# Kernel optimization log

Measured on AMD Instinct MI355X. Metric: run time of the kernel, lower is better.

## Reference

```python
import jax, jax.numpy as jnp
import numpy as np

NEG_SLOPE = 0.01  # F.leaky_relu default


def gcn_conv(x, src, dst, W, b):
    """PyG GCNConv: add self-loops, symmetric D^-1/2 (A+I) D^-1/2 normalization."""
    N = x.shape[0]
    loops = jnp.arange(N, dtype=src.dtype)
    src_f = jnp.concatenate([src, loops])  # [E+N]
    dst_f = jnp.concatenate([dst, loops])
    # degree counted on target nodes (includes self-loop), >= 1
    deg = jax.ops.segment_sum(jnp.ones_like(dst_f, dtype=x.dtype), dst_f, num_segments=N)
    dis = jax.lax.rsqrt(deg)  # deg >= 1 so finite
    norm = dis[src_f] * dis[dst_f]  # [E+N]
    h = x @ W  # [N, F_out] linear first (PyG order)
    msg = h[src_f] * norm[:, None]
    out = jax.ops.segment_sum(msg, dst_f, num_segments=N)
    return out + b


def setup_inputs() -> dict:
    key = jax.random.key(0)
    ks = jax.random.split(key, 8)
    N, E = 10000, 320000
    F_in, F1, F2 = 512, 256, 128
    x = jax.random.normal(ks[0], (N, F_in), dtype=jnp.float32)
    edge_index = jax.random.randint(ks[1], (2, E), 0, N, dtype=jnp.int32)
    batch = jnp.zeros((N,), dtype=jnp.int32)
    # Glorot-style params
    W1 = jax.random.normal(ks[2], (F_in, F1), dtype=jnp.float32) * (1.0 / np.sqrt(F_in))
    b1 = jnp.zeros((F1,), dtype=jnp.float32)
    W2 = jax.random.normal(ks[3], (F1, F2), dtype=jnp.float32) * (1.0 / np.sqrt(F1))
    b2 = jnp.zeros((F2,), dtype=jnp.float32)
    return {"x": x, "edge_index": edge_index, "batch": batch,
            "W1": W1, "b1": b1, "W2": W2, "b2": b2}


def reference(x, edge_index, batch, W1, b1, W2, b2):
    src, dst = edge_index[0], edge_index[1]
    h = jax.nn.leaky_relu(gcn_conv(x, src, dst, W1, b1), NEG_SLOPE)
    # dropout is eval-mode identity
    h = jax.nn.leaky_relu(gcn_conv(h, src, dst, W2, b2), NEG_SLOPE)
    x1 = jax.nn.sigmoid(h @ h.T)  # [N, N] dense decode
    return (x1, h)
```

## Files before the change

### kernel.cpp

```cpp
#include <hip/hip_runtime.h>
#include <math.h>

#define LEAKY 0.01f

using short8   = __attribute__((ext_vector_type(8))) short;
using f32x4    = __attribute__((ext_vector_type(4))) float;
using ushort4e = __attribute__((ext_vector_type(4))) unsigned short;

__device__ __forceinline__ ushort f2bf(float f) {
  uint u = __float_as_uint(f);
  uint r = (u + 0x7FFFu + ((u >> 16) & 1u)) >> 16;
  return (ushort)r;
}
__device__ __forceinline__ float bf2f(ushort h) {
  uint u = ((uint)h) << 16;
  return __uint_as_float(u);
}


__global__ void k_zero_i(int* __restrict__ p, int n) {
  int i = blockIdx.x * blockDim.x + threadIdx.x;
  if (i < n) p[i] = 0;
}

__global__ void k_count(const int* __restrict__ dst, int* __restrict__ cnt, int E) {
  int i = blockIdx.x * blockDim.x + threadIdx.x;
  if (i < E) atomicAdd(&cnt[dst[i]], 1);
}

__global__ void k_scan(const int* __restrict__ cnt, int* __restrict__ rowstart,
                       int* __restrict__ cursor, float* __restrict__ dinv,
                       int N, int Etot) {
  __shared__ int part[1024];
  const int t = threadIdx.x;
  const int CH = 16;
  int base = t * CH;
  int local[CH];
  int s = 0;
#pragma unroll
  for (int i = 0; i < CH; i++) {
    int v = (base + i < N) ? cnt[base + i] : 0;
    if (base + i < N) dinv[base + i] = rsqrtf((float)v + 1.0f);
    local[i] = s;
    s += v;
  }
  part[t] = s;
  __syncthreads();
  for (int off = 1; off < 1024; off <<= 1) {
    int add = (t >= off) ? part[t - off] : 0;
    __syncthreads();
    part[t] += add;
    __syncthreads();
  }
  int excl = (t == 0) ? 0 : part[t - 1];
#pragma unroll
  for (int i = 0; i < CH; i++) {
    if (base + i < N) {
      int rs = excl + local[i];
      rowstart[base + i] = rs;
      cursor[base + i] = rs;
    }
  }
  if (t == 0) rowstart[N] = Etot;
}

__global__ void k_csr(const int* __restrict__ src, const int* __restrict__ dst,
                      int* __restrict__ cursor, int* __restrict__ esrc, int E) {
  int i = blockIdx.x * blockDim.x + threadIdx.x;
  if (i < E) {
    int d = dst[i];
    int pos = atomicAdd(&cursor[d], 1);
    esrc[pos] = src[i];
  }
}


__global__ void k_xb(const float* __restrict__ X, ushort* __restrict__ Xb, long total) {
  long i = ((long)blockIdx.x * blockDim.x + threadIdx.x) * 4;
  if (i < total) {
    float4 v = *reinterpret_cast<const float4*>(&X[i]);
    ushort4e u = {f2bf(v.x), f2bf(v.y), f2bf(v.z), f2bf(v.w)};
    *reinterpret_cast<ushort4e*>(&Xb[i]) = u;
  }
}

__global__ void k_wt(const float* __restrict__ W1, ushort* __restrict__ Wt1,
                     int K1, int N1,
                     const float* __restrict__ W2, ushort* __restrict__ Wt2,
                     int K2, int N2) {
  int i = blockIdx.x * blockDim.x + threadIdx.x;
  int t1 = K1 * N1;
  if (i < t1) {
    int k = i / N1, n = i % N1;
    Wt1[(long)n * K1 + k] = f2bf(W1[i]);
  } else if (i < t1 + K2 * N2) {
    int j = i - t1;
    int k = j / N2, n = j % N2;
    Wt2[(long)n * K2 + k] = f2bf(W2[j]);
  }
}

template <int F, int VL, bool LAST>
__global__ __launch_bounds__(64) void k_agg(const ushort* __restrict__ hlin,
                                            const float* __restrict__ dinv,
                                            const int* __restrict__ rowstart,
                                            const int* __restrict__ esrc,
                                            const float* __restrict__ bias,
                                            ushort* __restrict__ aggb,
                                            float* __restrict__ outh, int N) {
  const int node = blockIdx.x;
  const int t = threadIdx.x;
  const float di = dinv[node];
  float acc[VL];
  {
    const ushort* p = hlin + (long)node * F + t * VL;
    if constexpr (VL == 4) {
      ushort4e v = *reinterpret_cast<const ushort4e*>(p);
#pragma unroll
      for (int i = 0; i < 4; i++) acc[i] = bf2f(v[i]) * di * di;
    } else {
      uint v = *reinterpret_cast<const uint*>(p);
      acc[0] = bf2f((ushort)(v & 0xffff)) * di * di;
      acc[1] = bf2f((ushort)(v >> 16)) * di * di;
    }
  }
  const int e0 = rowstart[node], e1 = rowstart[node + 1];
  int e = e0;
  for (; e + 3 < e1; e += 4) {
    int s0 = esrc[e], s1 = esrc[e + 1], s2 = esrc[e + 2], s3 = esrc[e + 3];
    float nm0 = dinv[s0] * di, nm1 = dinv[s1] * di;
    float nm2 = dinv[s2] * di, nm3 = dinv[s3] * di;
    const ushort* p0 = hlin + (long)s0 * F + t * VL;
    const ushort* p1 = hlin + (long)s1 * F + t * VL;
    const ushort* p2 = hlin + (long)s2 * F + t * VL;
    const ushort* p3 = hlin + (long)s3 * F + t * VL;
    if constexpr (VL == 4) {
      ushort4e v0 = *reinterpret_cast<const ushort4e*>(p0);
      ushort4e v1 = *reinterpret_cast<const ushort4e*>(p1);
      ushort4e v2 = *reinterpret_cast<const ushort4e*>(p2);
      ushort4e v3 = *reinterpret_cast<const ushort4e*>(p3);
#pragma unroll
      for (int i = 0; i < 4; i++)
        acc[i] += bf2f(v0[i]) * nm0 + bf2f(v1[i]) * nm1 +
                  bf2f(v2[i]) * nm2 + bf2f(v3[i]) * nm3;
    } else {
      uint v0 = *reinterpret_cast<const uint*>(p0);
      uint v1 = *reinterpret_cast<const uint*>(p1);
      uint v2 = *reinterpret_cast<const uint*>(p2);
      uint v3 = *reinterpret_cast<const uint*>(p3);
      acc[0] += bf2f((ushort)(v0 & 0xffff)) * nm0 + bf2f((ushort)(v1 & 0xffff)) * nm1 +
                bf2f((ushort)(v2 & 0xffff)) * nm2 + bf2f((ushort)(v3 & 0xffff)) * nm3;
      acc[1] += bf2f((ushort)(v0 >> 16)) * nm0 + bf2f((ushort)(v1 >> 16)) * nm1 +
                bf2f((ushort)(v2 >> 16)) * nm2 + bf2f((ushort)(v3 >> 16)) * nm3;
    }
  }
  for (; e < e1; e++) {
    int s0 = esrc[e];
    float nm0 = dinv[s0] * di;
    const ushort* p0 = hlin + (long)s0 * F + t * VL;
    if constexpr (VL == 4) {
      ushort4e v0 = *reinterpret_cast<const ushort4e*>(p0);
#pragma unroll
      for (int i = 0; i < 4; i++) acc[i] += bf2f(v0[i]) * nm0;
    } else {
      uint v0 = *reinterpret_cast<const uint*>(p0);
      acc[0] += bf2f((ushort)(v0 & 0xffff)) * nm0;
      acc[1] += bf2f((ushort)(v0 >> 16)) * nm0;
    }
  }
#pragma unroll
  for (int i = 0; i < VL; i++) {
    float v = acc[i] + bias[t * VL + i];
    acc[i] = (v > 0.f) ? v : (LEAKY * v);
  }
  if constexpr (VL == 4) {
    ushort4e o = {f2bf(acc[0]), f2bf(acc[1]), f2bf(acc[2]), f2bf(acc[3])};
    *reinterpret_cast<ushort4e*>(&aggb[(long)node * F + t * 4]) = o;
    if constexpr (LAST) {
      float4 fo = make_float4(acc[0], acc[1], acc[2], acc[3]);
      *reinterpret_cast<float4*>(&outh[(long)node * F + t * 4]) = fo;
    }
  } else {
    uint o = (uint)f2bf(acc[0]) | ((uint)f2bf(acc[1]) << 16);
    *reinterpret_cast<uint*>(&aggb[(long)node * F + t * 2]) = o;
    if constexpr (LAST) {
      float2 fo = make_float2(acc[0], acc[1]);
      *reinterpret_cast<float2*>(&outh[(long)node * F + t * 2]) = fo;
    }
  }
}

template <int BM>
__global__ __launch_bounds__(256) void k_gemm_bt(const ushort* __restrict__ Ab,
                                                 const ushort* __restrict__ Bb,
                                                 ushort* __restrict__ Cb,
                                                 int M, int N, int K, int ldc) {
  constexpr int MI = BM / 32;
  __shared__ __align__(16) ushort lds[(BM + 128) * 128];
  ushort* ldsA = lds;
  ushort* ldsB = lds + BM * 128;

  const int tid = threadIdx.x;
  const int lane = tid & 63;
  const int wv = tid >> 6;
  const int wr = wv >> 1, wc = wv & 1;
  const long bm = (long)blockIdx.y * BM;
  const long bn = (long)blockIdx.x * 128;

  f32x4 acc[MI][4];
#pragma unroll
  for (int i = 0; i < MI; i++)
#pragma unroll
    for (int j = 0; j < 4; j++) acc[i][j] = (f32x4){0.f, 0.f, 0.f, 0.f};

  const int kb = ((lane >> 4) << 4);

  for (int k0 = 0; k0 < K; k0 += 128) {
#pragma unroll
    for (int it = 0; it < BM / 16; it++) {
      int off = it * 4096 + tid * 16;
      int row = off >> 8;
      int cb = off & 255;
      long gr = bm + row;
      uint4 v = make_uint4(0u, 0u, 0u, 0u);
      if (gr < M) v = *reinterpret_cast<const uint4*>(&Ab[gr * K + k0 + (cb >> 1)]);
      int sb = (row << 8) | (cb ^ ((row & 7) << 4));
      *reinterpret_cast<uint4*>((char*)ldsA + sb) = v;
    }
#pragma unroll
    for (int it = 0; it < 8; it++) {
      int off = it * 4096 + tid * 16;
      int row = off >> 8;
      int cb = off & 255;
      long gn = bn + row;
      uint4 v = make_uint4(0u, 0u, 0u, 0u);
      if (gn < N) v = *reinterpret_cast<const uint4*>(&Bb[gn * K + k0 + (cb >> 1)]);
      int sb = (row << 8) | (cb ^ ((row & 7) << 4));
      *reinterpret_cast<uint4*>((char*)ldsB + sb) = v;
    }
    __syncthreads();

#pragma unroll
    for (int ks = 0; ks < 4; ks++) {
      short8 af[MI], bfr[4];
#pragma unroll
      for (int mi = 0; mi < MI; mi++) {
        int row = wr * (BM / 2) + mi * 16 + (lane & 15);
        int b = ks * 64 + kb;
        int addr = (row << 8) | (b ^ ((row & 7) << 4));
        af[mi] = *reinterpret_cast<const short8*>((const char*)ldsA + addr);
      }
#pragma unroll
      for (int ni = 0; ni < 4; ni++) {
        int row = wc * 64 + ni * 16 + (lane & 15);
        int b = ks * 64 + kb;
        int addr = (row << 8) | (b ^ ((row & 7) << 4));
        bfr[ni] = *reinterpret_cast<const short8*>((const char*)ldsB + addr);
      }
#pragma unroll
      for (int mi = 0; mi < MI; mi++)
#pragma unroll
        for (int ni = 0; ni < 4; ni++)
          acc[mi][ni] = __builtin_amdgcn_mfma_f32_16x16x32_bf16(af[mi], bfr[ni], acc[mi][ni], 0, 0, 0);
    }
    __syncthreads();
  }

#pragma unroll
  for (int ni = 0; ni < 4; ni++) {
    long col = bn + wc * 64 + ni * 16 + (lane & 15);
    if (col >= N) continue;
#pragma unroll
    for (int mi = 0; mi < MI; mi++) {
      long rbase2 = bm + wr * (BM / 2) + mi * 16 + ((lane >> 4) << 2);
#pragma unroll
      for (int j = 0; j < 4; j++) {
        long row = rbase2 + j;
        if (row >= M) continue;
        Cb[row * ldc + col] = f2bf(acc[mi][ni][j]);
      }
    }
  }
}

__global__ __launch_bounds__(256) void k_decode_sym(const ushort* __restrict__ Hb,
                                                    float* __restrict__ C, int N) {
  __shared__ __align__(16) ushort lds[2 * 128 * 128];
  ushort* ldsA = lds;
  ushort* ldsB = lds + 128 * 128;

  const int tid = threadIdx.x;
  const int lane = tid & 63;
  const int wv = tid >> 6;
  const int wr = wv >> 1, wc = wv & 1;

  int t = blockIdx.x;
  int bi = (int)((sqrtf(8.f * (float)t + 1.f) - 1.f) * 0.5f);
  while ((bi + 1) * (bi + 2) / 2 <= t) bi++;
  while (bi * (bi + 1) / 2 > t) bi--;
  int bj = t - bi * (bi + 1) / 2;
  const long bm = (long)bi * 128;
  const long bn = (long)bj * 128;

#pragma unroll
  for (int s = 0; s < 2; s++) {
    long rbase = s ? bn : bm;
    ushort* L = s ? ldsB : ldsA;
#pragma unroll
    for (int it = 0; it < 8; it++) {
      int off = it * 4096 + tid * 16;
      int row = off >> 8;
      int cb = off & 255;
      long grow = rbase + row;
      uint4 v = make_uint4(0u, 0u, 0u, 0u);
      if (grow < N)
        v = *reinterpret_cast<const uint4*>(&Hb[grow * 128 + (cb >> 1)]);
      int sb = (row << 8) | (cb ^ ((row & 7) << 4));
      *reinterpret_cast<uint4*>((char*)L + sb) = v;
    }
  }
  __syncthreads();

  f32x4 acc[4][4];
#pragma unroll
  for (int i = 0; i < 4; i++)
#pragma unroll
    for (int j = 0; j < 4; j++) acc[i][j] = (f32x4){0.f, 0.f, 0.f, 0.f};

  const int kb = ((lane >> 4) << 4);
#pragma unroll
  for (int ks = 0; ks < 4; ks++) {
    short8 af[4], bfr[4];
#pragma unroll
    for (int mi = 0; mi < 4; mi++) {
      int row = wr * 64 + mi * 16 + (lane & 15);
      int b = ks * 64 + kb;
      int addr = (row << 8) | (b ^ ((row & 7) << 4));
      af[mi] = *reinterpret_cast<const short8*>((const char*)ldsA + addr);
    }
#pragma unroll
    for (int ni = 0; ni < 4; ni++) {
      int row = wc * 64 + ni * 16 + (lane & 15);
      int b = ks * 64 + kb;
      int addr = (row << 8) | (b ^ ((row & 7) << 4));
      bfr[ni] = *reinterpret_cast<const short8*>((const char*)ldsB + addr);
    }
#pragma unroll
    for (int mi = 0; mi < 4; mi++)
#pragma unroll
      for (int ni = 0; ni < 4; ni++)
        acc[mi][ni] = __builtin_amdgcn_mfma_f32_16x16x32_bf16(af[mi], bfr[ni], acc[mi][ni], 0, 0, 0);
  }

#pragma unroll
  for (int mi = 0; mi < 4; mi++)
#pragma unroll
    for (int ni = 0; ni < 4; ni++)
#pragma unroll
      for (int j = 0; j < 4; j++)
        acc[mi][ni][j] = __builtin_amdgcn_rcpf(1.f + __expf(-acc[mi][ni][j]));

  if (bi != bj) {
#pragma unroll
    for (int ni = 0; ni < 4; ni++) {
      long gr = bn + wc * 64 + ni * 16 + (lane & 15);
#pragma unroll
      for (int mi = 0; mi < 4; mi++) {
        long gc = bm + wr * 64 + mi * 16 + ((lane >> 4) << 2);
        if (gr < N && gc < N)
          __builtin_nontemporal_store(acc[mi][ni],
                                      reinterpret_cast<f32x4*>(&C[gr * N + gc]));
      }
    }
  }

  __syncthreads();

  float* ft = (float*)lds;
#pragma unroll
  for (int ni = 0; ni < 4; ni++) {
    int col = wc * 64 + ni * 16 + (lane & 15);
#pragma unroll
    for (int mi = 0; mi < 4; mi++) {
      int rb = wr * 64 + mi * 16 + ((lane >> 4) << 2);
#pragma unroll
      for (int j = 0; j < 4; j++) {
        int row = rb + j;
        int byte = (row << 9) + (col << 2);
        byte ^= ((row & 7) << 4);
        *reinterpret_cast<float*>((char*)ft + byte) = acc[mi][ni][j];
      }
    }
  }
  __syncthreads();

#pragma unroll
  for (int it = 0; it < 16; it++) {
    int r = (tid >> 5) + it * 8;
    int ch = tid & 31;
    int byte = (r << 9) + (ch << 4);
    byte ^= ((r & 7) << 4);
    f32x4 v = *reinterpret_cast<const f32x4*>((const char*)ft + byte);
    long gr = bm + r;
    long gc = bn + ch * 4;
    if (gr < N && gc < N)
      __builtin_nontemporal_store(v, reinterpret_cast<f32x4*>(&C[gr * N + gc]));
  }
}


extern "C" void kernel_launch(void* const* d_in, const int* in_sizes, int n_in,
                              void* d_out, int out_size, void* d_ws, size_t ws_size,
                              hipStream_t stream) {
  const float* x  = (const float*)d_in[0];
  const int*   ei = (const int*)d_in[1];
  const float* W1 = (const float*)d_in[3];
  const float* b1 = (const float*)d_in[4];
  const float* W2 = (const float*)d_in[5];
  const float* b2 = (const float*)d_in[6];

  const int N   = in_sizes[2];
  const int E   = in_sizes[1] / 2;
  const int Fin = in_sizes[0] / N;
  const int F1  = in_sizes[4];
  const int F2  = in_sizes[6];

  const int* src = ei;
  const int* dst = ei + E;

  float* ws = (float*)d_ws;
  ushort* w1t      = (ushort*)ws;
  ushort* w2t      = (ushort*)(ws + 65536);
  ushort* xb       = (ushort*)(ws + 81920);
  ushort* h1b      = (ushort*)(ws + 2641920);
  ushort* agg1b    = (ushort*)(ws + 3921920);
  ushort* h2b      = (ushort*)(ws + 5201920);
  ushort* hb       = (ushort*)(ws + 5841920);
  float*  dinv     = ws + 6481920;
  int*    cnt      = (int*)(ws + 6492160);
  int*    cursor   = (int*)(ws + 6502400);
  int*    rowstart = (int*)(ws + 6512640);
  int*    esrc     = (int*)(ws + 6523136);

  float* out_x1 = (float*)d_out;
  float* out_h  = out_x1 + (long)N * N;

  k_zero_i<<<(N + 255) / 256, 256, 0, stream>>>(cnt, N);
  k_count<<<(E + 255) / 256, 256, 0, stream>>>(dst, cnt, E);
  k_scan<<<1, 1024, 0, stream>>>(cnt, rowstart, cursor, dinv, N, E);
  k_csr<<<(E + 255) / 256, 256, 0, stream>>>(src, dst, cursor, esrc, E);

  {
    int tot = Fin * F1 + F1 * F2;
    k_wt<<<(tot + 255) / 256, 256, 0, stream>>>(W1, w1t, Fin, F1, W2, w2t, F1, F2);
    long xtot = (long)N * Fin;
    k_xb<<<(unsigned)((xtot / 4 + 255) / 256), 256, 0, stream>>>(x, xb, xtot);
  }

  {
    dim3 grid(F1 / 128, (N + 63) / 64);
    k_gemm_bt<64><<<grid, 256, 0, stream>>>(xb, w1t, h1b, N, F1, Fin, F1);
  }
  k_agg<256, 4, false><<<N, 64, 0, stream>>>(h1b, dinv, rowstart, esrc, b1,
                                             agg1b, nullptr, N);

  {
    dim3 grid(F2 / 128, (N + 63) / 64);
    k_gemm_bt<64><<<grid, 256, 0, stream>>>(agg1b, w2t, h2b, N, F2, F1, F2);
  }
  k_agg<128, 2, true><<<N, 64, 0, stream>>>(h2b, dinv, rowstart, esrc, b2,
                                            hb, out_h, N);

  {
    int NB = (N + 127) / 128;
    int nblk = NB * (NB + 1) / 2;
    k_decode_sym<<<nblk, 256, 0, stream>>>(hb, out_x1, N);
  }
}
```

Before: 252.5 us.

## Precompute edge norms in CSR build, merge prep kernels, widen aggregation blocks

The CSR build now also stores a per-edge normalization (dinv[src]*dinv[dst]) in CSR order, so aggregation reads one float per edge instead of gathering dinv per neighbor. The X cast and weight-transpose kernels are merged into one launch, and the zeroing kernel is replaced by hipMemsetAsync. The aggregation kernel is reworked to use 2-feature lanes with multiple waves per node for the 256-wide layer and an 8-way unroll. This adds an E-sized float buffer and more threads per block in layer 1, but the dense decode likely dominates total time.

```diff
diff --git a/kernel.cpp b/kernel.cpp
--- a/kernel.cpp
+++ b/kernel.cpp
@@ -17,11 +17,6 @@
   return __uint_as_float(u);
 }
 
-
-__global__ void k_zero_i(int* __restrict__ p, int n) {
-  int i = blockIdx.x * blockDim.x + threadIdx.x;
-  if (i < n) p[i] = 0;
-}
 
 __global__ void k_count(const int* __restrict__ dst, int* __restrict__ cnt, int E) {
   int i = blockIdx.x * blockDim.x + threadIdx.x;
@@ -65,128 +60,96 @@
 }
 
 __global__ void k_csr(const int* __restrict__ src, const int* __restrict__ dst,
-                      int* __restrict__ cursor, int* __restrict__ esrc, int E) {
+                      const float* __restrict__ dinv, int* __restrict__ cursor,
+                      int* __restrict__ esrc, float* __restrict__ enorm, int E) {
   int i = blockIdx.x * blockDim.x + threadIdx.x;
   if (i < E) {
     int d = dst[i];
+    int s = src[i];
     int pos = atomicAdd(&cursor[d], 1);
-    esrc[pos] = src[i];
-  }
-}
-
-
-__global__ void k_xb(const float* __restrict__ X, ushort* __restrict__ Xb, long total) {
-  long i = ((long)blockIdx.x * blockDim.x + threadIdx.x) * 4;
-  if (i < total) {
-    float4 v = *reinterpret_cast<const float4*>(&X[i]);
+    esrc[pos] = s;
+    enorm[pos] = dinv[s] * dinv[d];
+  }
+}
+
+__global__ void k_prep(const float* __restrict__ X, ushort* __restrict__ Xb, long xq,
+                       const float* __restrict__ W1, ushort* __restrict__ Wt1,
+                       int K1, int N1,
+                       const float* __restrict__ W2, ushort* __restrict__ Wt2,
+                       int K2, int N2) {
+  long i = (long)blockIdx.x * blockDim.x + threadIdx.x;
+  if (i < xq) {
+    long b = i * 4;
+    float4 v = *reinterpret_cast<const float4*>(&X[b]);
     ushort4e u = {f2bf(v.x), f2bf(v.y), f2bf(v.z), f2bf(v.w)};
-    *reinterpret_cast<ushort4e*>(&Xb[i]) = u;
-  }
-}
-
-__global__ void k_wt(const float* __restrict__ W1, ushort* __restrict__ Wt1,
-                     int K1, int N1,
-                     const float* __restrict__ W2, ushort* __restrict__ Wt2,
-                     int K2, int N2) {
-  int i = blockIdx.x * blockDim.x + threadIdx.x;
-  int t1 = K1 * N1;
-  if (i < t1) {
-    int k = i / N1, n = i % N1;
-    Wt1[(long)n * K1 + k] = f2bf(W1[i]);
-  } else if (i < t1 + K2 * N2) {
-    int j = i - t1;
-    int k = j / N2, n = j % N2;
-    Wt2[(long)n * K2 + k] = f2bf(W2[j]);
-  }
-}
-
-template <int F, int VL, bool LAST>
-__global__ __launch_bounds__(64) void k_agg(const ushort* __restrict__ hlin,
-                                            const float* __restrict__ dinv,
-                                            const int* __restrict__ rowstart,
-                                            const int* __restrict__ esrc,
-                                            const float* __restrict__ bias,
-                                            ushort* __restrict__ aggb,
-                                            float* __restrict__ outh, int N) {
+    *reinterpret_cast<ushort4e*>(&Xb[b]) = u;
+  } else {
+    long j = i - xq;
+    int t1 = K1 * N1;
+    if (j < t1) {
+      int k = (int)(j / N1), n = (int)(j % N1);
+      Wt1[(long)n * K1 + k] = f2bf(W1[j]);
+    } else if (j < t1 + (long)K2 * N2) {
+      long jj = j - t1;
+      int k = (int)(jj / N2), n = (int)(jj % N2);
+      Wt2[(long)n * K2 + k] = f2bf(W2[jj]);
+    }
+  }
+}
+
+template <int F, int WAVES, bool LAST>
+__global__ __launch_bounds__(64 * WAVES) void k_agg(const ushort* __restrict__ hlin,
+                                                    const float* __restrict__ dinv,
+                                                    const int* __restrict__ rowstart,
+                                                    const int* __restrict__ esrc,
+                                                    const float* __restrict__ enorm,
+                                                    const float* __restrict__ bias,
+                                                    ushort* __restrict__ aggb,
+                                                    float* __restrict__ outh, int N) {
+  constexpr int FS = F / WAVES;
   const int node = blockIdx.x;
-  const int t = threadIdx.x;
+  const int tid = threadIdx.x;
+  const int w = tid >> 6;
+  const int lane = tid & 63;
+  const int f0 = w * FS + lane * 2;
   const float di = dinv[node];
-  float acc[VL];
+
+  float acc0, acc1;
   {
-    const ushort* p = hlin + (long)node * F + t * VL;
-    if constexpr (VL == 4) {
-      ushort4e v = *reinterpret_cast<const ushort4e*>(p);
-#pragma unroll
-      for (int i = 0; i < 4; i++) acc[i] = bf2f(v[i]) * di * di;
-    } else {
-      uint v = *reinterpret_cast<const uint*>(p);
-      acc[0] = bf2f((ushort)(v & 0xffff)) * di * di;
-      acc[1] = bf2f((ushort)(v >> 16)) * di * di;
-    }
+    uint v = *reinterpret_cast<const uint*>(&hlin[(long)node * F + f0]);
+    float dd = di * di;
+    acc0 = bf2f((ushort)(v & 0xffff)) * dd;
+    acc1 = bf2f((ushort)(v >> 16)) * dd;
   }
   const int e0 = rowstart[node], e1 = rowstart[node + 1];
   int e = e0;
-  for (; e + 3 < e1; e += 4) {
-    int s0 = esrc[e], s1 = esrc[e + 1], s2 = esrc[e + 2], s3 = esrc[e + 3];
-    float nm0 = dinv[s0] * di, nm1 = dinv[s1] * di;
-    float nm2 = dinv[s2] * di, nm3 = dinv[s3] * di;
-    const ushort* p0 = hlin + (long)s0 * F + t * VL;
-    const ushort* p1 = hlin + (long)s1 * F + t * VL;
-    const ushort* p2 = hlin + (long)s2 * F + t * VL;
-    const ushort* p3 = hlin + (long)s3 * F + t * VL;
-    if constexpr (VL == 4) {
-      ushort4e v0 = *reinterpret_cast<const ushort4e*>(p0);
-      ushort4e v1 = *reinterpret_cast<const ushort4e*>(p1);
-      ushort4e v2 = *reinterpret_cast<const ushort4e*>(p2);
-      ushort4e v3 = *reinterpret_cast<const ushort4e*>(p3);
-#pragma unroll
-      for (int i = 0; i < 4; i++)
-        acc[i] += bf2f(v0[i]) * nm0 + bf2f(v1[i]) * nm1 +
-                  bf2f(v2[i]) * nm2 + bf2f(v3[i]) * nm3;
-    } else {
-      uint v0 = *reinterpret_cast<const uint*>(p0);
-      uint v1 = *reinterpret_cast<const uint*>(p1);
-      uint v2 = *reinterpret_cast<const uint*>(p2);
-      uint v3 = *reinterpret_cast<const uint*>(p3);
-      acc[0] += bf2f((ushort)(v0 & 0xffff)) * nm0 + bf2f((ushort)(v1 & 0xffff)) * nm1 +
-                bf2f((ushort)(v2 & 0xffff)) * nm2 + bf2f((ushort)(v3 & 0xffff)) * nm3;
-      acc[1] += bf2f((ushort)(v0 >> 16)) * nm0 + bf2f((ushort)(v1 >> 16)) * nm1 +
-                bf2f((ushort)(v2 >> 16)) * nm2 + bf2f((ushort)(v3 >> 16)) * nm3;
+  for (; e + 7 < e1; e += 8) {
+#pragma unroll
+    for (int u = 0; u < 8; u++) {
+      int s = esrc[e + u];
+      float nm = enorm[e + u];
+      uint v = *reinterpret_cast<const uint*>(&hlin[(long)s * F + f0]);
+      acc0 += bf2f((ushort)(v & 0xffff)) * nm;
+      acc1 += bf2f((ushort)(v >> 16)) * nm;
     }
   }
   for (; e < e1; e++) {
-    int s0 = esrc[e];
-    float nm0 = dinv[s0] * di;
-    const ushort* p0 = hlin + (long)s0 * F + t * VL;
-    if constexpr (VL == 4) {
-      ushort4e v0 = *reinterpret_cast<const ushort4e*>(p0);
-#pragma unroll
-      for (int i = 0; i < 4; i++) acc[i] += bf2f(v0[i]) * nm0;
-    } else {
-      uint v0 = *reinterpret_cast<const uint*>(p0);
-      acc[0] += bf2f((ushort)(v0 & 0xffff)) * nm0;
-      acc[1] += bf2f((ushort)(v0 >> 16)) * nm0;
-    }
-  }
-#pragma unroll
-  for (int i = 0; i < VL; i++) {
-    float v = acc[i] + bias[t * VL + i];
-    acc[i] = (v > 0.f) ? v : (LEAKY * v);
-  }
-  if constexpr (VL == 4) {
-    ushort4e o = {f2bf(acc[0]), f2bf(acc[1]), f2bf(acc[2]), f2bf(acc[3])};
-    *reinterpret_cast<ushort4e*>(&aggb[(long)node * F + t * 4]) = o;
-    if constexpr (LAST) {
-      float4 fo = make_float4(acc[0], acc[1], acc[2], acc[3]);
-      *reinterpret_cast<float4*>(&outh[(long)node * F + t * 4]) = fo;
-    }
-  } else {
-    uint o = (uint)f2bf(acc[0]) | ((uint)f2bf(acc[1]) << 16);
-    *reinterpret_cast<uint*>(&aggb[(long)node * F + t * 2]) = o;
-    if constexpr (LAST) {
-      float2 fo = make_float2(acc[0], acc[1]);
-      *reinterpret_cast<float2*>(&outh[(long)node * F + t * 2]) = fo;
-    }
+    int s = esrc[e];
+    float nm = enorm[e];
+    uint v = *reinterpret_cast<const uint*>(&hlin[(long)s * F + f0]);
+    acc0 += bf2f((ushort)(v & 0xffff)) * nm;
+    acc1 += bf2f((ushort)(v >> 16)) * nm;
+  }
+
+  float v0 = acc0 + bias[f0];
+  float v1 = acc1 + bias[f0 + 1];
+  v0 = (v0 > 0.f) ? v0 : (LEAKY * v0);
+  v1 = (v1 > 0.f) ? v1 : (LEAKY * v1);
+  uint o = (uint)f2bf(v0) | ((uint)f2bf(v1) << 16);
+  *reinterpret_cast<uint*>(&aggb[(long)node * F + f0]) = o;
+  if constexpr (LAST) {
+    float2 fo = make_float2(v0, v1);
+    *reinterpret_cast<float2*>(&outh[(long)node * F + f0]) = fo;
   }
 }
 
@@ -441,34 +404,35 @@
   int*    cursor   = (int*)(ws + 6502400);
   int*    rowstart = (int*)(ws + 6512640);
   int*    esrc     = (int*)(ws + 6523136);
+  float*  enorm    = ws + 6843136;
 
   float* out_x1 = (float*)d_out;
   float* out_h  = out_x1 + (long)N * N;
 
-  k_zero_i<<<(N + 255) / 256, 256, 0, stream>>>(cnt, N);
+  hipMemsetAsync(cnt, 0, (size_t)N * sizeof(int), stream);
   k_count<<<(E + 255) / 256, 256, 0, stream>>>(dst, cnt, E);
   k_scan<<<1, 1024, 0, stream>>>(cnt, rowstart, cursor, dinv, N, E);
-  k_csr<<<(E + 255) / 256, 256, 0, stream>>>(src, dst, cursor, esrc, E);
+  k_csr<<<(E + 255) / 256, 256, 0, stream>>>(src, dst, dinv, cursor, esrc, enorm, E);
 
   {
-    int tot = Fin * F1 + F1 * F2;
-    k_wt<<<(tot + 255) / 256, 256, 0, stream>>>(W1, w1t, Fin, F1, W2, w2t, F1, F2);
-    long xtot = (long)N * Fin;
-    k_xb<<<(unsigned)((xtot / 4 + 255) / 256), 256, 0, stream>>>(x, xb, xtot);
+    long xq = (long)N * Fin / 4;
+    long tot = xq + (long)Fin * F1 + (long)F1 * F2;
+    k_prep<<<(unsigned)((tot + 255) / 256), 256, 0, stream>>>(
+        x, xb, xq, W1, w1t, Fin, F1, W2, w2t, F1, F2);
   }
 
   {
     dim3 grid(F1 / 128, (N + 63) / 64);
     k_gemm_bt<64><<<grid, 256, 0, stream>>>(xb, w1t, h1b, N, F1, Fin, F1);
   }
-  k_agg<256, 4, false><<<N, 64, 0, stream>>>(h1b, dinv, rowstart, esrc, b1,
-                                             agg1b, nullptr, N);
+  k_agg<256, 2, false><<<N, 128, 0, stream>>>(h1b, dinv, rowstart, esrc, enorm, b1,
+                                              agg1b, nullptr, N);
 
   {
     dim3 grid(F2 / 128, (N + 63) / 64);
     k_gemm_bt<64><<<grid, 256, 0, stream>>>(agg1b, w2t, h2b, N, F2, F1, F2);
   }
-  k_agg<128, 2, true><<<N, 64, 0, stream>>>(h2b, dinv, rowstart, esrc, b2,
+  k_agg<128, 1, true><<<N, 64, 0, stream>>>(h2b, dinv, rowstart, esrc, enorm, b2,
                                             hb, out_h, N);
 
   {
```

After: 248.3 us. No clear change (-1.7%).
